# Optimization experiments

Hardware: AMD Instinct MI355X
Metric: run time of the kernel (lower is better)

The kernel has to match this reference:

```python
import jax, jax.numpy as jnp
import numpy as np
from jax.ops import segment_sum

IN_DIM, HID_DIM, OUT_DIM = 128, 128, 64
N_NODES, N_EDGES = 50000, 800000


def gcn_conv(x, src, dst, W, b, n_nodes):
    # Symmetric GCN normalization (no self loops): deg at targets from unit weights
    deg = segment_sum(jnp.ones(src.shape[0], dtype=x.dtype), dst, num_segments=n_nodes)
    dinv = jnp.where(deg > 0, jax.lax.rsqrt(jnp.maximum(deg, 1.0)), 0.0)
    norm = dinv[src] * dinv[dst]                      # [E]
    h = x @ W                                         # [N, out] small GEMM first (PyG order)
    msg = h[src] * norm[:, None]                      # gather + scale: [E, out]
    out = segment_sum(msg, dst, num_segments=n_nodes) # scatter-add to targets
    return out + b


def setup_inputs() -> dict:
    key = jax.random.key(0)
    k1, k2, k3, k4, k5 = jax.random.split(key, 5)
    x = jax.random.normal(k1, (N_NODES, IN_DIM), dtype=jnp.float32)
    edge_index = jax.random.randint(k2, (2, N_EDGES), 0, N_NODES, dtype=jnp.int64)
    s1 = 1.0 / np.sqrt(IN_DIM)
    s2 = 1.0 / np.sqrt(HID_DIM)
    W1 = jax.random.uniform(k3, (IN_DIM, HID_DIM), jnp.float32, -s1, s1)
    b1 = jnp.zeros((HID_DIM,), jnp.float32)
    W2 = jax.random.uniform(k4, (HID_DIM, OUT_DIM), jnp.float32, -s2, s2)
    b2 = jnp.zeros((OUT_DIM,), jnp.float32)
    return {"x": x, "edge_index": edge_index, "W1": W1, "b1": b1, "W2": W2, "b2": b2}


def reference(x, edge_index, W1, b1, W2, b2):
    n_nodes = x.shape[0]
    src, dst = edge_index[0], edge_index[1]
    h = gcn_conv(x, src, dst, W1, b1, n_nodes)
    h = jax.nn.relu(h)
    # Dropout is identity in eval mode (reference is deterministic)
    out = gcn_conv(h, src, dst, W2, b2, n_nodes)
    return out
```

## Files before the change

### kernel.cpp

```cpp
#include <hip/hip_runtime.h>

#define N_NODES 50000
#define N_EDGES 800000
#define IN_DIM  128
#define HID_DIM 128
#define OUT_DIM 64

#define NPAD 50176
#define CAP  64
#define GEMM1B ((N_NODES + 63) / 64)
#define RANKB (N_EDGES / 256)
#define PREPB 24

typedef __attribute__((ext_vector_type(8))) short bf16x8;
typedef __attribute__((ext_vector_type(4))) float f32x4;

__device__ __forceinline__ unsigned short f2bf(float f) {
    unsigned u = __float_as_uint(f);
    u += 0x7fffu + ((u >> 16) & 1u);
    return (unsigned short)(u >> 16);
}
__device__ __forceinline__ float bflo(unsigned u) { return __uint_as_float(u << 16); }
__device__ __forceinline__ float bfhi(unsigned u) { return __uint_as_float(u & 0xffff0000u); }

#define ACC8(u)  do { \
    acc[0] += bflo(u.x); acc[1] += bfhi(u.x); \
    acc[2] += bflo(u.y); acc[3] += bfhi(u.y); \
    acc[4] += bflo(u.z); acc[5] += bfhi(u.z); \
    acc[6] += bflo(u.w); acc[7] += bfhi(u.w); } while (0)


__global__ __launch_bounds__(256) void prep_fill_kernel(const int* __restrict__ src,
                                                        const int* __restrict__ dst,
                                                        int* __restrict__ cnt,
                                                        unsigned short* __restrict__ csr_src,
                                                        const float* __restrict__ W1,
                                                        const float* __restrict__ W2,
                                                        unsigned short* __restrict__ w1t,
                                                        unsigned short* __restrict__ w2t) {
    int bid = blockIdx.x;
    int tid = threadIdx.x;
    if (bid < 16) {
        int idx = bid * 256 + tid;
        int c = idx >> 5, k4 = (idx & 31) * 4;
        ushort4 o;
        o.x = f2bf(W1[(k4 + 0) * 128 + c]);
        o.y = f2bf(W1[(k4 + 1) * 128 + c]);
        o.z = f2bf(W1[(k4 + 2) * 128 + c]);
        o.w = f2bf(W1[(k4 + 3) * 128 + c]);
        *(ushort4*)(w1t + c * 128 + k4) = o;
    } else if (bid < PREPB) {
        int idx = (bid - 16) * 256 + tid;
        int c = idx >> 5, k4 = (idx & 31) * 4;
        ushort4 o;
        o.x = f2bf(W2[(k4 + 0) * 64 + c]);
        o.y = f2bf(W2[(k4 + 1) * 64 + c]);
        o.z = f2bf(W2[(k4 + 2) * 64 + c]);
        o.w = f2bf(W2[(k4 + 3) * 64 + c]);
        *(ushort4*)(w2t + c * 128 + k4) = o;
    } else {
        int e = (bid - PREPB) * 256 + tid;
        int s = src[e], d = dst[e];
        int slot = atomicAdd(&cnt[d], 1);
        if (slot < CAP) csr_src[(d << 6) + slot] = (unsigned short)s;
    }
}


__global__ __launch_bounds__(256) void gemm1_kernel(const float* __restrict__ x,
                                                    const unsigned short* __restrict__ w1t,
                                                    const int* __restrict__ cnt,
                                                    float* __restrict__ dinv,
                                                    unsigned short* __restrict__ h1b) {
    int gb = blockIdx.x;
    int wave = threadIdx.x >> 6;
    int lane = threadIdx.x & 63;
    int n = lane & 15, quad = lane >> 4;
    int row0 = gb * 64 + wave * 16;

    int arow = row0 + n;
    if (arow >= N_NODES) arow = N_NODES - 1;
    const float* aptr = x + (size_t)arow * 128 + quad * 8;
    const unsigned short* bbase = w1t + (size_t)n * 128 + quad * 8;

    f32x4 acc[8];
#pragma unroll
    for (int t = 0; t < 8; ++t) acc[t] = (f32x4){0.f, 0.f, 0.f, 0.f};

#pragma unroll
    for (int w4 = 0; w4 < 4; ++w4) {
        float4 f0 = *(const float4*)(aptr + w4 * 32);
        float4 f1 = *(const float4*)(aptr + w4 * 32 + 4);
        bf16x8 af;
        af[0] = (short)f2bf(f0.x); af[1] = (short)f2bf(f0.y);
        af[2] = (short)f2bf(f0.z); af[3] = (short)f2bf(f0.w);
        af[4] = (short)f2bf(f1.x); af[5] = (short)f2bf(f1.y);
        af[6] = (short)f2bf(f1.z); af[7] = (short)f2bf(f1.w);
#pragma unroll
        for (int t = 0; t < 8; ++t) {
            bf16x8 bf = *(const bf16x8*)(bbase + (size_t)t * 2048 + w4 * 32);
            acc[t] = __builtin_amdgcn_mfma_f32_16x16x32_bf16(af, bf, acc[t], 0, 0, 0);
        }
    }

#pragma unroll
    for (int r = 0; r < 4; ++r) {
        int row = row0 + quad * 4 + r;
        if (row < N_NODES) {
            int deg = cnt[row];
            float dn = (deg > 0) ? rsqrtf((float)deg) : 0.0f;
            if (n == 0) dinv[row] = dn;
            unsigned short* o = h1b + (size_t)row * 128 + n;
#pragma unroll
            for (int t = 0; t < 8; ++t) o[t * 16] = f2bf(acc[t][r] * dn);
        }
    }
}


#define A1T_STRIDE 136

__global__ __launch_bounds__(256) void agg1_gemm2_fused(const unsigned short* __restrict__ csr_src,
                                                        const int* __restrict__ cnt,
                                                        const float* __restrict__ dinv,
                                                        const float* __restrict__ b1,
                                                        const unsigned short* __restrict__ h1b,
                                                        const unsigned short* __restrict__ w2t,
                                                        unsigned short* __restrict__ h2b) {
    __shared__ unsigned short a1t[16 * A1T_STRIDE];

    int node0 = blockIdx.x * 16;
    int g = threadIdx.x >> 4;
    int q = threadIdx.x & 15;
    int node = node0 + g;
    int start = node << 6;
    int m = cnt[node];
    if (m > CAP) m = CAP;

    float acc[8] = {};
    int j = 0;
    for (; j + 7 < m; j += 8) {
        ushort4 sa = *(const ushort4*)(csr_src + start + j);
        ushort4 sb = *(const ushort4*)(csr_src + start + j + 4);
        uint4 u0 = ((const uint4*)(h1b + (size_t)sa.x * 128))[q];
        uint4 u1 = ((const uint4*)(h1b + (size_t)sa.y * 128))[q];
        uint4 u2 = ((const uint4*)(h1b + (size_t)sa.z * 128))[q];
        uint4 u3 = ((const uint4*)(h1b + (size_t)sa.w * 128))[q];
        uint4 u4 = ((const uint4*)(h1b + (size_t)sb.x * 128))[q];
        uint4 u5 = ((const uint4*)(h1b + (size_t)sb.y * 128))[q];
        uint4 u6 = ((const uint4*)(h1b + (size_t)sb.z * 128))[q];
        uint4 u7 = ((const uint4*)(h1b + (size_t)sb.w * 128))[q];
        ACC8(u0); ACC8(u1); ACC8(u2); ACC8(u3);
        ACC8(u4); ACC8(u5); ACC8(u6); ACC8(u7);
    }
    for (; j + 3 < m; j += 4) {
        ushort4 sa = *(const ushort4*)(csr_src + start + j);
        uint4 u0 = ((const uint4*)(h1b + (size_t)sa.x * 128))[q];
        uint4 u1 = ((const uint4*)(h1b + (size_t)sa.y * 128))[q];
        uint4 u2 = ((const uint4*)(h1b + (size_t)sa.z * 128))[q];
        uint4 u3 = ((const uint4*)(h1b + (size_t)sa.w * 128))[q];
        ACC8(u0); ACC8(u1); ACC8(u2); ACC8(u3);
    }
    for (; j < m; ++j) {
        int s0 = csr_src[start + j];
        uint4 u0 = ((const uint4*)(h1b + (size_t)s0 * 128))[q];
        ACC8(u0);
    }

    {
        float dn = dinv[node];
        float4 bA = ((const float4*)b1)[2 * q];
        float4 bB = ((const float4*)b1)[2 * q + 1];
        ushort4 oA, oB;
        oA.x = f2bf(fmaxf(acc[0] * dn + bA.x, 0.f));
        oA.y = f2bf(fmaxf(acc[1] * dn + bA.y, 0.f));
        oA.z = f2bf(fmaxf(acc[2] * dn + bA.z, 0.f));
        oA.w = f2bf(fmaxf(acc[3] * dn + bA.w, 0.f));
        oB.x = f2bf(fmaxf(acc[4] * dn + bB.x, 0.f));
        oB.y = f2bf(fmaxf(acc[5] * dn + bB.y, 0.f));
        oB.z = f2bf(fmaxf(acc[6] * dn + bB.z, 0.f));
        oB.w = f2bf(fmaxf(acc[7] * dn + bB.w, 0.f));
        ushort4* o = (ushort4*)(a1t + g * A1T_STRIDE + q * 8);
        o[0] = oA;
        o[1] = oB;
    }
    __syncthreads();

    int wave = threadIdx.x >> 6;
    int lane = threadIdx.x & 63;
    int n = lane & 15, quad = lane >> 4;
    const unsigned short* bbase = w2t + (size_t)(wave * 16 + n) * 128 + quad * 8;
    const unsigned short* abase = a1t + (size_t)n * A1T_STRIDE + quad * 8;

    f32x4 c2 = (f32x4){0.f, 0.f, 0.f, 0.f};
#pragma unroll
    for (int w4 = 0; w4 < 4; ++w4) {
        bf16x8 af = *(const bf16x8*)(abase + w4 * 32);
        bf16x8 bf = *(const bf16x8*)(bbase + w4 * 32);
        c2 = __builtin_amdgcn_mfma_f32_16x16x32_bf16(af, bf, c2, 0, 0, 0);
    }

#pragma unroll
    for (int r = 0; r < 4; ++r) {
        int row = node0 + quad * 4 + r;
        float dn = dinv[row];
        h2b[(size_t)row * 64 + wave * 16 + n] = f2bf(c2[r] * dn);
    }
}


__global__ __launch_bounds__(256) void agg2_kernel(const unsigned short* __restrict__ csr_src,
                                                   const int* __restrict__ cnt,
                                                   const float* __restrict__ dinv,
                                                   const float* __restrict__ b2,
                                                   const unsigned short* __restrict__ h2b,
                                                   float* __restrict__ out) {
    int node = blockIdx.x * 4 + (threadIdx.x >> 6);
    if (node >= N_NODES) return;
    int lane = threadIdx.x & 63;
    int grp = lane >> 3;
    int q   = lane & 7;
    int start = node << 6;
    int m = cnt[node];
    if (m > CAP) m = CAP;

    float acc[8] = {};

    int j = grp;
    for (; j + 8 < m; j += 16) {
        int s0 = csr_src[start + j];
        int s1 = csr_src[start + j + 8];
        uint4 u0 = ((const uint4*)(h2b + (size_t)s0 * 64))[q];
        uint4 u1 = ((const uint4*)(h2b + (size_t)s1 * 64))[q];
        ACC8(u0); ACC8(u1);
    }
    if (j < m) {
        int s0 = csr_src[start + j];
        uint4 u0 = ((const uint4*)(h2b + (size_t)s0 * 64))[q];
        ACC8(u0);
    }

#pragma unroll
    for (int d = 8; d <= 32; d <<= 1) {
#pragma unroll
        for (int c = 0; c < 8; ++c) acc[c] += __shfl_xor(acc[c], d, 64);
    }

    if (lane < 8) {
        float dn = dinv[node];
        float4 bA = ((const float4*)b2)[2 * q];
        float4 bB = ((const float4*)b2)[2 * q + 1];
        float4 rA, rB;
        rA.x = acc[0] * dn + bA.x;
        rA.y = acc[1] * dn + bA.y;
        rA.z = acc[2] * dn + bA.z;
        rA.w = acc[3] * dn + bA.w;
        rB.x = acc[4] * dn + bB.x;
        rB.y = acc[5] * dn + bB.y;
        rB.z = acc[6] * dn + bB.z;
        rB.w = acc[7] * dn + bB.w;
        float4* o = (float4*)(out + (size_t)node * 64);
        o[2 * q] = rA;
        o[2 * q + 1] = rB;
    }
}


extern "C" void kernel_launch(void* const* d_in, const int* in_sizes, int n_in,
                              void* d_out, int out_size, void* d_ws, size_t ws_size,
                              hipStream_t stream) {
    const float* x  = (const float*)d_in[0];
    const int*   ei = (const int*)d_in[1];
    const float* W1 = (const float*)d_in[2];
    const float* b1 = (const float*)d_in[3];
    const float* W2 = (const float*)d_in[4];
    const float* b2 = (const float*)d_in[5];
    float* out = (float*)d_out;

    const int* src = ei;
    const int* dst = ei + N_EDGES;

    char* ws = (char*)d_ws;
    int*   cnt       = (int*)ws;
    float* dinv      = (float*)(cnt + NPAD);
    unsigned short* csr_src = (unsigned short*)(dinv + NPAD);
    unsigned short* h1b = csr_src + (size_t)N_NODES * CAP;
    unsigned short* h2b = h1b + (size_t)N_NODES * HID_DIM;
    unsigned short* w1t = h2b + (size_t)N_NODES * OUT_DIM;
    unsigned short* w2t = w1t + 128 * 128;

    (void)hipMemsetAsync(cnt, 0, NPAD * sizeof(int), stream);

    prep_fill_kernel<<<PREPB + RANKB, 256, 0, stream>>>(src, dst, cnt, csr_src,
                                                        W1, W2, w1t, w2t);

    gemm1_kernel<<<GEMM1B, 256, 0, stream>>>(x, w1t, cnt, dinv, h1b);

    agg1_gemm2_fused<<<N_NODES / 16, 256, 0, stream>>>(csr_src, cnt, dinv, b1, h1b, w2t, h2b);

    agg2_kernel<<<(N_NODES + 3) / 4, 256, 0, stream>>>(csr_src, cnt, dinv, b2, h2b, out);
}
```

Measured before the change: 203.4 us.

## Merge CSR fill with GEMM1, move source-degree scaling into aggregation

The memset moves into a small init kernel that also transposes the weights. The CSR fill and the first GEMM now run as one launch with independent block ranges, because GEMM1 no longer needs degrees: its output is left unscaled. The source-side normalization moves into the first aggregation as per-neighbor cnt lookups plus an rsqrt, and dinv is recomputed from cnt wherever it is needed instead of being stored. This removes one launch and the memset in exchange for an extra random gather and rsqrt per edge in agg1.

```diff
diff --git a/kernel.cpp b/kernel.cpp
--- a/kernel.cpp
+++ b/kernel.cpp
@@ -9,8 +9,8 @@
 #define NPAD 50176
 #define CAP  64
 #define GEMM1B ((N_NODES + 63) / 64)
-#define RANKB (N_EDGES / 256)
-#define PREPB 24
+#define FILLB (N_EDGES / 256)
+#define INITB 24
 
 typedef __attribute__((ext_vector_type(8))) short bf16x8;
 typedef __attribute__((ext_vector_type(4))) float f32x4;
@@ -29,15 +29,22 @@
     acc[4] += bflo(u.z); acc[5] += bfhi(u.z); \
     acc[6] += bflo(u.w); acc[7] += bfhi(u.w); } while (0)
 
-
-__global__ __launch_bounds__(256) void prep_fill_kernel(const int* __restrict__ src,
-                                                        const int* __restrict__ dst,
-                                                        int* __restrict__ cnt,
-                                                        unsigned short* __restrict__ csr_src,
-                                                        const float* __restrict__ W1,
-                                                        const float* __restrict__ W2,
-                                                        unsigned short* __restrict__ w1t,
-                                                        unsigned short* __restrict__ w2t) {
+#define FMA8(u, sc_)  do { \
+    acc[0] += bflo(u.x) * (sc_); acc[1] += bfhi(u.x) * (sc_); \
+    acc[2] += bflo(u.y) * (sc_); acc[3] += bfhi(u.y) * (sc_); \
+    acc[4] += bflo(u.z) * (sc_); acc[5] += bfhi(u.z) * (sc_); \
+    acc[6] += bflo(u.w) * (sc_); acc[7] += bfhi(u.w) * (sc_); } while (0)
+
+__device__ __forceinline__ float deg2dinv(int deg) {
+    return (deg > 0) ? rsqrtf((float)deg) : 0.0f;
+}
+
+
+__global__ __launch_bounds__(256) void init_kernel(const float* __restrict__ W1,
+                                                   const float* __restrict__ W2,
+                                                   unsigned short* __restrict__ w1t,
+                                                   unsigned short* __restrict__ w2t,
+                                                   int* __restrict__ cnt) {
     int bid = blockIdx.x;
     int tid = threadIdx.x;
     if (bid < 16) {
@@ -49,7 +56,7 @@
         o.z = f2bf(W1[(k4 + 2) * 128 + c]);
         o.w = f2bf(W1[(k4 + 3) * 128 + c]);
         *(ushort4*)(w1t + c * 128 + k4) = o;
-    } else if (bid < PREPB) {
+    } else {
         int idx = (bid - 16) * 256 + tid;
         int c = idx >> 5, k4 = (idx & 31) * 4;
         ushort4 o;
@@ -58,21 +65,30 @@
         o.z = f2bf(W2[(k4 + 2) * 64 + c]);
         o.w = f2bf(W2[(k4 + 3) * 64 + c]);
         *(ushort4*)(w2t + c * 128 + k4) = o;
-    } else {
-        int e = (bid - PREPB) * 256 + tid;
+    }
+    int4 z = {0, 0, 0, 0};
+    for (int i = bid * 256 + tid; i < NPAD / 4; i += INITB * 256)
+        ((int4*)cnt)[i] = z;
+}
+
+
+__global__ __launch_bounds__(256) void fill_gemm1_kernel(const int* __restrict__ src,
+                                                         const int* __restrict__ dst,
+                                                         int* __restrict__ cnt,
+                                                         unsigned short* __restrict__ csr_src,
+                                                         const float* __restrict__ x,
+                                                         const unsigned short* __restrict__ w1t,
+                                                         unsigned short* __restrict__ h1b) {
+    int bid = blockIdx.x;
+    if (bid < FILLB) {
+        int e = bid * 256 + threadIdx.x;
         int s = src[e], d = dst[e];
         int slot = atomicAdd(&cnt[d], 1);
         if (slot < CAP) csr_src[(d << 6) + slot] = (unsigned short)s;
-    }
-}
-
-
-__global__ __launch_bounds__(256) void gemm1_kernel(const float* __restrict__ x,
-                                                    const unsigned short* __restrict__ w1t,
-                                                    const int* __restrict__ cnt,
-                                                    float* __restrict__ dinv,
-                                                    unsigned short* __restrict__ h1b) {
-    int gb = blockIdx.x;
+        return;
+    }
+
+    int gb = bid - FILLB;
     int wave = threadIdx.x >> 6;
     int lane = threadIdx.x & 63;
     int n = lane & 15, quad = lane >> 4;
@@ -107,12 +123,9 @@
     for (int r = 0; r < 4; ++r) {
         int row = row0 + quad * 4 + r;
         if (row < N_NODES) {
-            int deg = cnt[row];
-            float dn = (deg > 0) ? rsqrtf((float)deg) : 0.0f;
-            if (n == 0) dinv[row] = dn;
             unsigned short* o = h1b + (size_t)row * 128 + n;
 #pragma unroll
-            for (int t = 0; t < 8; ++t) o[t * 16] = f2bf(acc[t][r] * dn);
+            for (int t = 0; t < 8; ++t) o[t * 16] = f2bf(acc[t][r]);
         }
     }
 }
@@ -122,7 +135,6 @@
 
 __global__ __launch_bounds__(256) void agg1_gemm2_fused(const unsigned short* __restrict__ csr_src,
                                                         const int* __restrict__ cnt,
-                                                        const float* __restrict__ dinv,
                                                         const float* __restrict__ b1,
                                                         const unsigned short* __restrict__ h1b,
                                                         const unsigned short* __restrict__ w2t,
@@ -135,6 +147,7 @@
     int node = node0 + g;
     int start = node << 6;
     int m = cnt[node];
+    float dn = deg2dinv(m);
     if (m > CAP) m = CAP;
 
     float acc[8] = {};
@@ -142,6 +155,14 @@
     for (; j + 7 < m; j += 8) {
         ushort4 sa = *(const ushort4*)(csr_src + start + j);
         ushort4 sb = *(const ushort4*)(csr_src + start + j + 4);
+        float d0 = deg2dinv(cnt[sa.x]);
+        float d1 = deg2dinv(cnt[sa.y]);
+        float d2 = deg2dinv(cnt[sa.z]);
+        float d3 = deg2dinv(cnt[sa.w]);
+        float d4 = deg2dinv(cnt[sb.x]);
+        float d5 = deg2dinv(cnt[sb.y]);
+        float d6 = deg2dinv(cnt[sb.z]);
+        float d7 = deg2dinv(cnt[sb.w]);
         uint4 u0 = ((const uint4*)(h1b + (size_t)sa.x * 128))[q];
         uint4 u1 = ((const uint4*)(h1b + (size_t)sa.y * 128))[q];
         uint4 u2 = ((const uint4*)(h1b + (size_t)sa.z * 128))[q];
@@ -150,25 +171,29 @@
         uint4 u5 = ((const uint4*)(h1b + (size_t)sb.y * 128))[q];
         uint4 u6 = ((const uint4*)(h1b + (size_t)sb.z * 128))[q];
         uint4 u7 = ((const uint4*)(h1b + (size_t)sb.w * 128))[q];
-        ACC8(u0); ACC8(u1); ACC8(u2); ACC8(u3);
-        ACC8(u4); ACC8(u5); ACC8(u6); ACC8(u7);
+        FMA8(u0, d0); FMA8(u1, d1); FMA8(u2, d2); FMA8(u3, d3);
+        FMA8(u4, d4); FMA8(u5, d5); FMA8(u6, d6); FMA8(u7, d7);
     }
     for (; j + 3 < m; j += 4) {
         ushort4 sa = *(const ushort4*)(csr_src + start + j);
+        float d0 = deg2dinv(cnt[sa.x]);
+        float d1 = deg2dinv(cnt[sa.y]);
+        float d2 = deg2dinv(cnt[sa.z]);
+        float d3 = deg2dinv(cnt[sa.w]);
         uint4 u0 = ((const uint4*)(h1b + (size_t)sa.x * 128))[q];
         uint4 u1 = ((const uint4*)(h1b + (size_t)sa.y * 128))[q];
         uint4 u2 = ((const uint4*)(h1b + (size_t)sa.z * 128))[q];
         uint4 u3 = ((const uint4*)(h1b + (size_t)sa.w * 128))[q];
-        ACC8(u0); ACC8(u1); ACC8(u2); ACC8(u3);
+        FMA8(u0, d0); FMA8(u1, d1); FMA8(u2, d2); FMA8(u3, d3);
     }
     for (; j < m; ++j) {
         int s0 = csr_src[start + j];
+        float d0 = deg2dinv(cnt[s0]);
         uint4 u0 = ((const uint4*)(h1b + (size_t)s0 * 128))[q];
-        ACC8(u0);
+        FMA8(u0, d0);
     }
 
     {
-        float dn = dinv[node];
         float4 bA = ((const float4*)b1)[2 * q];
         float4 bB = ((const float4*)b1)[2 * q + 1];
         ushort4 oA, oB;
@@ -203,15 +228,14 @@
 #pragma unroll
     for (int r = 0; r < 4; ++r) {
         int row = node0 + quad * 4 + r;
-        float dn = dinv[row];
-        h2b[(size_t)row * 64 + wave * 16 + n] = f2bf(c2[r] * dn);
+        float dr = deg2dinv(cnt[row]);
+        h2b[(size_t)row * 64 + wave * 16 + n] = f2bf(c2[r] * dr);
     }
 }
 
 
 __global__ __launch_bounds__(256) void agg2_kernel(const unsigned short* __restrict__ csr_src,
                                                    const int* __restrict__ cnt,
-                                                   const float* __restrict__ dinv,
                                                    const float* __restrict__ b2,
                                                    const unsigned short* __restrict__ h2b,
                                                    float* __restrict__ out) {
@@ -222,6 +246,7 @@
     int q   = lane & 7;
     int start = node << 6;
     int m = cnt[node];
+    float dn = deg2dinv(m);
     if (m > CAP) m = CAP;
 
     float acc[8] = {};
@@ -247,7 +272,6 @@
     }
 
     if (lane < 8) {
-        float dn = dinv[node];
         float4 bA = ((const float4*)b2)[2 * q];
         float4 bB = ((const float4*)b2)[2 * q + 1];
         float4 rA, rB;
@@ -282,21 +306,18 @@
 
     char* ws = (char*)d_ws;
     int*   cnt       = (int*)ws;
-    float* dinv      = (float*)(cnt + NPAD);
-    unsigned short* csr_src = (unsigned short*)(dinv + NPAD);
+    unsigned short* csr_src = (unsigned short*)(cnt + NPAD);
     unsigned short* h1b = csr_src + (size_t)N_NODES * CAP;
     unsigned short* h2b = h1b + (size_t)N_NODES * HID_DIM;
     unsigned short* w1t = h2b + (size_t)N_NODES * OUT_DIM;
     unsigned short* w2t = w1t + 128 * 128;
 
-    (void)hipMemsetAsync(cnt, 0, NPAD * sizeof(int), stream);
-
-    prep_fill_kernel<<<PREPB + RANKB, 256, 0, stream>>>(src, dst, cnt, csr_src,
-                                                        W1, W2, w1t, w2t);
-
-    gemm1_kernel<<<GEMM1B, 256, 0, stream>>>(x, w1t, cnt, dinv, h1b);
-
-    agg1_gemm2_fused<<<N_NODES / 16, 256, 0, stream>>>(csr_src, cnt, dinv, b1, h1b, w2t, h2b);
-
-    agg2_kernel<<<(N_NODES + 3) / 4, 256, 0, stream>>>(csr_src, cnt, dinv, b2, h2b, out);
-}
+    init_kernel<<<INITB, 256, 0, stream>>>(W1, W2, w1t, w2t, cnt);
+
+    fill_gemm1_kernel<<<FILLB + GEMM1B, 256, 0, stream>>>(src, dst, cnt, csr_src,
+                                                          x, w1t, h1b);
+
+    agg1_gemm2_fused<<<N_NODES / 16, 256, 0, stream>>>(csr_src, cnt, b1, h1b, w2t, h2b);
+
+    agg2_kernel<<<(N_NODES + 3) / 4, 256, 0, stream>>>(csr_src, cnt, b2, h2b, out);
+}
```

Result: slower. 215.8 us (+6.1%).

## Split bf16 feature matrices into 64-byte column planes and recompute dinv inline

Applied to the files above, without the earlier changes.

Stores h1 and h2 as separate column planes of 32 bf16 values each, so every gathered neighbor row is one 64-byte segment per plane. The aggregation kernels loop over planes and spread edges across lanes, reducing the partial sums with shuffles. The goal is a smaller gather footprint per pass, which should give better cache locality on the random-access gathers. The dinv buffer is also removed and recomputed from the counts with rsqrt. In exchange, every plane pass re-reads the CSR indices and adds cross-lane shuffle reductions.

```diff
diff --git a/kernel.cpp b/kernel.cpp
--- a/kernel.cpp
+++ b/kernel.cpp
@@ -9,8 +9,10 @@
 #define NPAD 50176
 #define CAP  64
 #define GEMM1B ((N_NODES + 63) / 64)
-#define RANKB (N_EDGES / 256)
+#define FILLB (N_EDGES / 256)
 #define PREPB 24
+#define PL1 (N_NODES * 32)
+#define PL2 (N_NODES * 32)
 
 typedef __attribute__((ext_vector_type(8))) short bf16x8;
 typedef __attribute__((ext_vector_type(4))) float f32x4;
@@ -28,6 +30,10 @@
     acc[2] += bflo(u.y); acc[3] += bfhi(u.y); \
     acc[4] += bflo(u.z); acc[5] += bfhi(u.z); \
     acc[6] += bflo(u.w); acc[7] += bfhi(u.w); } while (0)
+
+__device__ __forceinline__ float deg2dinv(int deg) {
+    return (deg > 0) ? rsqrtf((float)deg) : 0.0f;
+}
 
 
 __global__ __launch_bounds__(256) void prep_fill_kernel(const int* __restrict__ src,
@@ -70,7 +76,6 @@
 __global__ __launch_bounds__(256) void gemm1_kernel(const float* __restrict__ x,
                                                     const unsigned short* __restrict__ w1t,
                                                     const int* __restrict__ cnt,
-                                                    float* __restrict__ dinv,
                                                     unsigned short* __restrict__ h1b) {
     int gb = blockIdx.x;
     int wave = threadIdx.x >> 6;
@@ -107,12 +112,11 @@
     for (int r = 0; r < 4; ++r) {
         int row = row0 + quad * 4 + r;
         if (row < N_NODES) {
-            int deg = cnt[row];
-            float dn = (deg > 0) ? rsqrtf((float)deg) : 0.0f;
-            if (n == 0) dinv[row] = dn;
-            unsigned short* o = h1b + (size_t)row * 128 + n;
-#pragma unroll
-            for (int t = 0; t < 8; ++t) o[t * 16] = f2bf(acc[t][r] * dn);
+            float dn = deg2dinv(cnt[row]);
+#pragma unroll
+            for (int t = 0; t < 8; ++t)
+                h1b[(size_t)(t >> 1) * PL1 + (size_t)row * 32 + n + 16 * (t & 1)]
+                    = f2bf(acc[t][r] * dn);
         }
     }
 }
@@ -122,7 +126,6 @@
 
 __global__ __launch_bounds__(256) void agg1_gemm2_fused(const unsigned short* __restrict__ csr_src,
                                                         const int* __restrict__ cnt,
-                                                        const float* __restrict__ dinv,
                                                         const float* __restrict__ b1,
                                                         const unsigned short* __restrict__ h1b,
                                                         const unsigned short* __restrict__ w2t,
@@ -130,59 +133,55 @@
     __shared__ unsigned short a1t[16 * A1T_STRIDE];
 
     int node0 = blockIdx.x * 16;
-    int g = threadIdx.x >> 4;
-    int q = threadIdx.x & 15;
+    int g  = threadIdx.x >> 4;
+    int r_ = threadIdx.x & 15;
+    int e4 = r_ >> 2;
+    int s  = r_ & 3;
     int node = node0 + g;
     int start = node << 6;
     int m = cnt[node];
+    float dn = deg2dinv(m);
     if (m > CAP) m = CAP;
 
-    float acc[8] = {};
-    int j = 0;
-    for (; j + 7 < m; j += 8) {
-        ushort4 sa = *(const ushort4*)(csr_src + start + j);
-        ushort4 sb = *(const ushort4*)(csr_src + start + j + 4);
-        uint4 u0 = ((const uint4*)(h1b + (size_t)sa.x * 128))[q];
-        uint4 u1 = ((const uint4*)(h1b + (size_t)sa.y * 128))[q];
-        uint4 u2 = ((const uint4*)(h1b + (size_t)sa.z * 128))[q];
-        uint4 u3 = ((const uint4*)(h1b + (size_t)sa.w * 128))[q];
-        uint4 u4 = ((const uint4*)(h1b + (size_t)sb.x * 128))[q];
-        uint4 u5 = ((const uint4*)(h1b + (size_t)sb.y * 128))[q];
-        uint4 u6 = ((const uint4*)(h1b + (size_t)sb.z * 128))[q];
-        uint4 u7 = ((const uint4*)(h1b + (size_t)sb.w * 128))[q];
-        ACC8(u0); ACC8(u1); ACC8(u2); ACC8(u3);
-        ACC8(u4); ACC8(u5); ACC8(u6); ACC8(u7);
-    }
-    for (; j + 3 < m; j += 4) {
-        ushort4 sa = *(const ushort4*)(csr_src + start + j);
-        uint4 u0 = ((const uint4*)(h1b + (size_t)sa.x * 128))[q];
-        uint4 u1 = ((const uint4*)(h1b + (size_t)sa.y * 128))[q];
-        uint4 u2 = ((const uint4*)(h1b + (size_t)sa.z * 128))[q];
-        uint4 u3 = ((const uint4*)(h1b + (size_t)sa.w * 128))[q];
-        ACC8(u0); ACC8(u1); ACC8(u2); ACC8(u3);
-    }
-    for (; j < m; ++j) {
-        int s0 = csr_src[start + j];
-        uint4 u0 = ((const uint4*)(h1b + (size_t)s0 * 128))[q];
-        ACC8(u0);
-    }
-
-    {
-        float dn = dinv[node];
-        float4 bA = ((const float4*)b1)[2 * q];
-        float4 bB = ((const float4*)b1)[2 * q + 1];
-        ushort4 oA, oB;
-        oA.x = f2bf(fmaxf(acc[0] * dn + bA.x, 0.f));
-        oA.y = f2bf(fmaxf(acc[1] * dn + bA.y, 0.f));
-        oA.z = f2bf(fmaxf(acc[2] * dn + bA.z, 0.f));
-        oA.w = f2bf(fmaxf(acc[3] * dn + bA.w, 0.f));
-        oB.x = f2bf(fmaxf(acc[4] * dn + bB.x, 0.f));
-        oB.y = f2bf(fmaxf(acc[5] * dn + bB.y, 0.f));
-        oB.z = f2bf(fmaxf(acc[6] * dn + bB.z, 0.f));
-        oB.w = f2bf(fmaxf(acc[7] * dn + bB.w, 0.f));
-        ushort4* o = (ushort4*)(a1t + g * A1T_STRIDE + q * 8);
-        o[0] = oA;
-        o[1] = oB;
+#pragma unroll
+    for (int p = 0; p < 4; ++p) {
+        const unsigned short* hp = h1b + (size_t)p * PL1;
+        float acc[8] = {};
+        int j = e4;
+        for (; j + 4 < m; j += 8) {
+            int s0 = csr_src[start + j];
+            int s1 = csr_src[start + j + 4];
+            uint4 u0 = *(const uint4*)(hp + (size_t)s0 * 32 + s * 8);
+            uint4 u1 = *(const uint4*)(hp + (size_t)s1 * 32 + s * 8);
+            ACC8(u0); ACC8(u1);
+        }
+        if (j < m) {
+            int s0 = csr_src[start + j];
+            uint4 u0 = *(const uint4*)(hp + (size_t)s0 * 32 + s * 8);
+            ACC8(u0);
+        }
+#pragma unroll
+        for (int c = 0; c < 8; ++c) {
+            acc[c] += __shfl_xor(acc[c], 4, 64);
+            acc[c] += __shfl_xor(acc[c], 8, 64);
+        }
+        if (e4 == 0) {
+            int c0 = p * 32 + s * 8;
+            float4 bA = *(const float4*)(b1 + c0);
+            float4 bB = *(const float4*)(b1 + c0 + 4);
+            ushort4 oA, oB;
+            oA.x = f2bf(fmaxf(acc[0] * dn + bA.x, 0.f));
+            oA.y = f2bf(fmaxf(acc[1] * dn + bA.y, 0.f));
+            oA.z = f2bf(fmaxf(acc[2] * dn + bA.z, 0.f));
+            oA.w = f2bf(fmaxf(acc[3] * dn + bA.w, 0.f));
+            oB.x = f2bf(fmaxf(acc[4] * dn + bB.x, 0.f));
+            oB.y = f2bf(fmaxf(acc[5] * dn + bB.y, 0.f));
+            oB.z = f2bf(fmaxf(acc[6] * dn + bB.z, 0.f));
+            oB.w = f2bf(fmaxf(acc[7] * dn + bB.w, 0.f));
+            ushort4* o = (ushort4*)(a1t + g * A1T_STRIDE + c0);
+            o[0] = oA;
+            o[1] = oB;
+        }
     }
     __syncthreads();
 
@@ -203,65 +202,61 @@
 #pragma unroll
     for (int r = 0; r < 4; ++r) {
         int row = node0 + quad * 4 + r;
-        float dn = dinv[row];
-        h2b[(size_t)row * 64 + wave * 16 + n] = f2bf(c2[r] * dn);
+        float dr = deg2dinv(cnt[row]);
+        h2b[(size_t)(wave >> 1) * PL2 + (size_t)row * 32 + (wave & 1) * 16 + n]
+            = f2bf(c2[r] * dr);
     }
 }
 
 
 __global__ __launch_bounds__(256) void agg2_kernel(const unsigned short* __restrict__ csr_src,
                                                    const int* __restrict__ cnt,
-                                                   const float* __restrict__ dinv,
                                                    const float* __restrict__ b2,
                                                    const unsigned short* __restrict__ h2b,
                                                    float* __restrict__ out) {
     int node = blockIdx.x * 4 + (threadIdx.x >> 6);
     if (node >= N_NODES) return;
     int lane = threadIdx.x & 63;
-    int grp = lane >> 3;
-    int q   = lane & 7;
+    int egrp = lane >> 2;
+    int s    = lane & 3;
     int start = node << 6;
     int m = cnt[node];
+    float dn = deg2dinv(m);
     if (m > CAP) m = CAP;
 
-    float acc[8] = {};
-
-    int j = grp;
-    for (; j + 8 < m; j += 16) {
-        int s0 = csr_src[start + j];
-        int s1 = csr_src[start + j + 8];
-        uint4 u0 = ((const uint4*)(h2b + (size_t)s0 * 64))[q];
-        uint4 u1 = ((const uint4*)(h2b + (size_t)s1 * 64))[q];
-        ACC8(u0); ACC8(u1);
-    }
-    if (j < m) {
-        int s0 = csr_src[start + j];
-        uint4 u0 = ((const uint4*)(h2b + (size_t)s0 * 64))[q];
-        ACC8(u0);
-    }
-
-#pragma unroll
-    for (int d = 8; d <= 32; d <<= 1) {
-#pragma unroll
-        for (int c = 0; c < 8; ++c) acc[c] += __shfl_xor(acc[c], d, 64);
-    }
-
-    if (lane < 8) {
-        float dn = dinv[node];
-        float4 bA = ((const float4*)b2)[2 * q];
-        float4 bB = ((const float4*)b2)[2 * q + 1];
-        float4 rA, rB;
-        rA.x = acc[0] * dn + bA.x;
-        rA.y = acc[1] * dn + bA.y;
-        rA.z = acc[2] * dn + bA.z;
-        rA.w = acc[3] * dn + bA.w;
-        rB.x = acc[4] * dn + bB.x;
-        rB.y = acc[5] * dn + bB.y;
-        rB.z = acc[6] * dn + bB.z;
-        rB.w = acc[7] * dn + bB.w;
-        float4* o = (float4*)(out + (size_t)node * 64);
-        o[2 * q] = rA;
-        o[2 * q + 1] = rB;
+#pragma unroll
+    for (int p = 0; p < 2; ++p) {
+        const unsigned short* hp = h2b + (size_t)p * PL2;
+        float acc[8] = {};
+        for (int j = egrp; j < m; j += 16) {
+            int s0 = csr_src[start + j];
+            uint4 u0 = *(const uint4*)(hp + (size_t)s0 * 32 + s * 8);
+            ACC8(u0);
+        }
+#pragma unroll
+        for (int c = 0; c < 8; ++c) {
+            acc[c] += __shfl_xor(acc[c], 4, 64);
+            acc[c] += __shfl_xor(acc[c], 8, 64);
+            acc[c] += __shfl_xor(acc[c], 16, 64);
+            acc[c] += __shfl_xor(acc[c], 32, 64);
+        }
+        if (lane < 4) {
+            int c0 = p * 32 + s * 8;
+            float4 bA = *(const float4*)(b2 + c0);
+            float4 bB = *(const float4*)(b2 + c0 + 4);
+            float4 rA, rB;
+            rA.x = acc[0] * dn + bA.x;
+            rA.y = acc[1] * dn + bA.y;
+            rA.z = acc[2] * dn + bA.z;
+            rA.w = acc[3] * dn + bA.w;
+            rB.x = acc[4] * dn + bB.x;
+            rB.y = acc[5] * dn + bB.y;
+            rB.z = acc[6] * dn + bB.z;
+            rB.w = acc[7] * dn + bB.w;
+            float4* o = (float4*)(out + (size_t)node * 64 + c0);
+            o[0] = rA;
+            o[1] = rB;
+        }
     }
 }
 
@@ -282,21 +277,20 @@
 
     char* ws = (char*)d_ws;
     int*   cnt       = (int*)ws;
-    float* dinv      = (float*)(cnt + NPAD);
-    unsigned short* csr_src = (unsigned short*)(dinv + NPAD);
+    unsigned short* csr_src = (unsigned short*)(cnt + NPAD);
     unsigned short* h1b = csr_src + (size_t)N_NODES * CAP;
-    unsigned short* h2b = h1b + (size_t)N_NODES * HID_DIM;
-    unsigned short* w1t = h2b + (size_t)N_NODES * OUT_DIM;
+    unsigned short* h2b = h1b + (size_t)4 * PL1;
+    unsigned short* w1t = h2b + (size_t)2 * PL2;
     unsigned short* w2t = w1t + 128 * 128;
 
     (void)hipMemsetAsync(cnt, 0, NPAD * sizeof(int), stream);
 
-    prep_fill_kernel<<<PREPB + RANKB, 256, 0, stream>>>(src, dst, cnt, csr_src,
+    prep_fill_kernel<<<PREPB + FILLB, 256, 0, stream>>>(src, dst, cnt, csr_src,
                                                         W1, W2, w1t, w2t);
 
-    gemm1_kernel<<<GEMM1B, 256, 0, stream>>>(x, w1t, cnt, dinv, h1b);
-
-    agg1_gemm2_fused<<<N_NODES / 16, 256, 0, stream>>>(csr_src, cnt, dinv, b1, h1b, w2t, h2b);
-
-    agg2_kernel<<<(N_NODES + 3) / 4, 256, 0, stream>>>(csr_src, cnt, dinv, b2, h2b, out);
-}
+    gemm1_kernel<<<GEMM1B, 256, 0, stream>>>(x, w1t, cnt, h1b);
+
+    agg1_gemm2_fused<<<N_NODES / 16, 256, 0, stream>>>(csr_src, cnt, b1, h1b, w2t, h2b);
+
+    agg2_kernel<<<(N_NODES + 3) / 4, 256, 0, stream>>>(csr_src, cnt, b2, h2b, out);
+}
```

Result: slower. 228.6 us (+12.4%).
